# Kernel optimization log

Measured on AMD Instinct MI355X. Metric: run time of the kernel, lower is better.

Reference implementation:

```python
import jax, jax.numpy as jnp
import numpy as np

R = 16
EPS = 1e-6
OFFSETS = (1, 2, 4, 8, 16, 32)
_IDX_I, _IDX_J = np.triu_indices(R, k=1)  # plu_dim = 120


def _plucker(u, v):
    # u, v: (B, L, r) -> (B, L, plu_dim), normalized with eps-clamped norm
    p = u[..., _IDX_I] * v[..., _IDX_J] - u[..., _IDX_J] * v[..., _IDX_I]
    norm = jnp.maximum(jnp.linalg.norm(p, axis=-1, keepdims=True), EPS)
    return p / norm


def setup_inputs() -> dict:
    key = jax.random.key(0)
    ks = jax.random.split(key, 6)
    B, L, D, d_geom = 4, 4096, 1024, 256
    plu_dim = R * (R - 1) // 2
    s = lambda fan_in: 1.0 / np.sqrt(fan_in)
    return {
        "h": jax.random.normal(ks[0], (B, L, D), jnp.float32),
        "red_w": jax.random.normal(ks[1], (D, R), jnp.float32) * s(D),
        "red_b": jnp.zeros((R,), jnp.float32),
        "g1_w": jax.random.normal(ks[2], (plu_dim, d_geom), jnp.float32) * s(plu_dim),
        "g1_b": jnp.zeros((d_geom,), jnp.float32),
        "g2_w": jax.random.normal(ks[3], (d_geom, D), jnp.float32) * s(d_geom),
        "g2_b": jnp.zeros((D,), jnp.float32),
        "gate_w": jax.random.normal(ks[4], (2 * D, D), jnp.float32) * s(2 * D),
        "gate_b": jnp.zeros((D,), jnp.float32),
    }


def reference(h, red_w, red_b, g1_w, g1_b, g2_w, g2_b, gate_w, gate_b):
    B, L, D = h.shape
    z = h @ red_w + red_b  # (B, L, r)
    geom_sum = jnp.zeros((B, L, D), h.dtype)
    count = jnp.zeros((B, L, 1), h.dtype)
    pos = jnp.arange(L)
    for delta in OFFSETS:
        if delta >= L:
            continue
        # causal shift: z_past[t] = z[t - delta], zero-padded
        z_past = jnp.pad(z[:, : L - delta], ((0, 0), (delta, 0), (0, 0)))
        p = _plucker(z_past, z)  # (B, L, plu_dim)
        g_delta = jax.nn.gelu(p @ g1_w + g1_b, approximate=False) @ g2_w + g2_b
        mask = (pos >= delta).astype(h.dtype)[None, :, None]  # (1, L, 1)
        geom_sum = geom_sum + g_delta * mask
        count = count + jnp.broadcast_to(mask, (B, L, 1))
    g = geom_sum / jnp.maximum(count, 1.0)
    alpha = jax.nn.sigmoid(jnp.concatenate([h, g], axis=-1) @ gate_w + gate_b)
    return alpha * h + (1.0 - alpha) * g
```

## Files before the change

### kernel.cpp

```cpp
#include <hip/hip_runtime.h>
#include <hip/hip_bf16.h>
#include <math.h>

typedef unsigned short u16;
typedef unsigned int u32;
typedef __attribute__((ext_vector_type(8))) short short8;
typedef __attribute__((ext_vector_type(4))) float f32x4;

#define L_SEQ 4096
#define N_TOK 16384
#define D_MODEL 1024
#define R_DIM 16
#define PLU 120
#define G_DIM 256
#define K_CAT 1536
#define K_GATE 2048

typedef __attribute__((address_space(1))) const void* as1cvp;
typedef __attribute__((address_space(3))) void* as3vp;
#define GLD16(g, l) \
  __builtin_amdgcn_global_load_lds((as1cvp)(g), (as3vp)(l), 16, 0, 0)

#define CFENCE asm volatile("" ::: "memory")
#define BARB                        \
  {                                 \
    CFENCE;                         \
    __builtin_amdgcn_s_barrier();   \
    CFENCE;                         \
  }
#define VM0 asm volatile("s_waitcnt vmcnt(0)" ::: "memory")

__device__ __forceinline__ u16 f2bf(float f) {
  u32 x = __float_as_uint(f);
  u32 lsb = (x >> 16) & 1u;
  x += 0x7fffu + lsb;
  return (u16)(x >> 16);
}
__device__ __forceinline__ float bf2f(u16 u) {
  return __uint_as_float(((u32)u) << 16);
}
__device__ __forceinline__ u32 pack2(float a, float b) {
  return (u32)f2bf(a) | ((u32)f2bf(b) << 16);
}

constexpr int PLU_I[PLU] = {
    0, 0, 0, 0, 0, 0, 0, 0, 0, 0, 0, 0, 0, 0, 0,
    1, 1, 1, 1, 1, 1, 1, 1, 1, 1, 1, 1, 1, 1,
    2, 2, 2, 2, 2, 2, 2, 2, 2, 2, 2, 2, 2,
    3, 3, 3, 3, 3, 3, 3, 3, 3, 3, 3, 3,
    4, 4, 4, 4, 4, 4, 4, 4, 4, 4, 4,
    5, 5, 5, 5, 5, 5, 5, 5, 5, 5,
    6, 6, 6, 6, 6, 6, 6, 6, 6,
    7, 7, 7, 7, 7, 7, 7, 7,
    8, 8, 8, 8, 8, 8, 8,
    9, 9, 9, 9, 9, 9,
    10, 10, 10, 10, 10,
    11, 11, 11, 11,
    12, 12, 12,
    13, 13,
    14};
constexpr int PLU_J[PLU] = {
    1, 2, 3, 4, 5, 6, 7, 8, 9, 10, 11, 12, 13, 14, 15,
    2, 3, 4, 5, 6, 7, 8, 9, 10, 11, 12, 13, 14, 15,
    3, 4, 5, 6, 7, 8, 9, 10, 11, 12, 13, 14, 15,
    4, 5, 6, 7, 8, 9, 10, 11, 12, 13, 14, 15,
    5, 6, 7, 8, 9, 10, 11, 12, 13, 14, 15,
    6, 7, 8, 9, 10, 11, 12, 13, 14, 15,
    7, 8, 9, 10, 11, 12, 13, 14, 15,
    8, 9, 10, 11, 12, 13, 14, 15,
    9, 10, 11, 12, 13, 14, 15,
    10, 11, 12, 13, 14, 15,
    11, 12, 13, 14, 15,
    12, 13, 14, 15,
    13, 14, 15,
    14, 15,
    15};

__global__ __launch_bounds__(256) void k_cvtT(const float* __restrict__ src,
                                              u16* __restrict__ dst, int K,
                                              int Kp, int N) {
  __shared__ float t[32][33];
  const int k0 = blockIdx.y * 32, n0 = blockIdx.x * 32;
  const int r = threadIdx.x >> 3, c4 = (threadIdx.x & 7) * 4;
  float4 v = {0.f, 0.f, 0.f, 0.f};
  if (k0 + r < K) v = *(const float4*)(src + (size_t)(k0 + r) * N + n0 + c4);
  t[r][c4] = v.x;
  t[r][c4 + 1] = v.y;
  t[r][c4 + 2] = v.z;
  t[r][c4 + 3] = v.w;
  __syncthreads();
  uint2 o;
  o.x = pack2(t[c4][r], t[c4 + 1][r]);
  o.y = pack2(t[c4 + 2][r], t[c4 + 3][r]);
  *(uint2*)(dst + (size_t)(n0 + r) * Kp + k0 + c4) = o;
}

__global__ __launch_bounds__(256) void k_reduce(const float* __restrict__ h,
                                                const float* __restrict__ red_w,
                                                const float* __restrict__ red_b,
                                                float* __restrict__ z,
                                                u16* __restrict__ hb) {
  __shared__ alignas(16) u16 hs[16 * D_MODEL];
  const int tid = threadIdx.x;
  const int t0 = blockIdx.x * 16;

  const float4* src = (const float4*)(h + (size_t)t0 * D_MODEL);
  u32* dst = (u32*)hs;
#pragma unroll
  for (int it = 0; it < (16 * D_MODEL / 4) / 256; ++it) {
    const int idx = tid + it * 256;
    const float4 v = src[idx];
    dst[idx * 2 + 0] = pack2(v.x, v.y);
    dst[idx * 2 + 1] = pack2(v.z, v.w);
  }
  __syncthreads();

  {
    const uint4* s4 = (const uint4*)hs;
    uint4* d4 = (uint4*)(hb + (size_t)t0 * D_MODEL);
#pragma unroll
    for (int it = 0; it < (16 * D_MODEL / 8) / 256; ++it)
      d4[tid + it * 256] = s4[tid + it * 256];
  }

  const int m = tid >> 4, c = tid & 15;
  const u16* hrow = hs + m * D_MODEL;
  float acc = 0.f;
#pragma unroll 8
  for (int i = 0; i < D_MODEL; i += 2) {
    u32 hv = *(const u32*)(hrow + i);
    float h0 = __uint_as_float(hv << 16);
    float h1 = __uint_as_float(hv & 0xffff0000u);
    acc = fmaf(h0, red_w[i * R_DIM + c], acc);
    acc = fmaf(h1, red_w[(i + 1) * R_DIM + c], acc);
  }
  z[(size_t)(t0 + m) * R_DIM + c] = acc + red_b[c];
}

__global__ __launch_bounds__(256) void k_plu(const float* __restrict__ z,
                                             const u16* __restrict__ W1t,
                                             const float* __restrict__ g1b,
                                             u16* __restrict__ A, int t0g) {
  __shared__ alignas(16) float zx[160][17];
  __shared__ alignas(16) u16 W1s[128][136];
  __shared__ alignas(16) u16 Pb[128][136];
  __shared__ float prt[128][2];
  __shared__ float rno[128];
  __shared__ float b1s[128];

  const int tid = threadIdx.x, lane = tid & 63, w = tid >> 6;
  const int wm = w >> 1, wn = w & 1;
  const int n0 = blockIdx.x * 128;
  const int tl = blockIdx.y * 128;
  const int tg = t0g + tl;
  const int l0 = tg & (L_SEQ - 1);
  const int kq = (lane >> 4) * 8, mr = lane & 15;

  if (tid < 128) b1s[tid] = g1b[n0 + tid];
  for (int r = tid; r < 160 * 16; r += 256) {
    const int rr = r >> 4, c = r & 15;
    int t = tg - 32 + rr;
    if (t < 0) t = 0;
    zx[rr][c] = z[(size_t)t * R_DIM + c];
  }
  {
    const uint4* src = (const uint4*)(W1t + (size_t)n0 * 128);
    for (int i = tid; i < 128 * 16; i += 256) {
      const int r = i >> 4, c = i & 15;
      *(uint4*)&W1s[r][c * 8] = src[i];
    }
  }

  f32x4 acc[4][4];

#pragma unroll 1
  for (int dd = 0; dd < 6; ++dd) {
    const int delta = 1 << dd;
    __syncthreads();
    {
      const int row = tid >> 1, half = tid & 1;
      const float* zc = zx[32 + row];
      const float* zpr = zx[32 + row - delta];
      float zcr[R_DIM], zpr_[R_DIM];
#pragma unroll
      for (int c = 0; c < R_DIM; ++c) {
        zcr[c] = zc[c];
        zpr_[c] = zpr[c];
      }
      float s = 0.f;
      u16* pb = &Pb[row][0];
      if (half == 0) {
#pragma unroll
        for (int k = 0; k < 60; ++k) {
          const float p = zpr_[PLU_I[k]] * zcr[PLU_J[k]] -
                          zpr_[PLU_J[k]] * zcr[PLU_I[k]];
          s = fmaf(p, p, s);
          pb[k] = f2bf(p);
        }
      } else {
#pragma unroll
        for (int k = 60; k < 120; ++k) {
          const float p = zpr_[PLU_I[k]] * zcr[PLU_J[k]] -
                          zpr_[PLU_J[k]] * zcr[PLU_I[k]];
          s = fmaf(p, p, s);
          pb[k] = f2bf(p);
        }
        uint4 zz = {0u, 0u, 0u, 0u};
        *(uint4*)&pb[120] = zz;
      }
      prt[row][half] = s;
    }
    __syncthreads();
    if (tid < 128) {
      const float s = prt[tid][0] + prt[tid][1];
      rno[tid] = 1.0f / fmaxf(sqrtf(s), 1e-6f);
    }
    __syncthreads();
#pragma unroll
    for (int a = 0; a < 4; ++a)
#pragma unroll
      for (int b = 0; b < 4; ++b) acc[a][b] = (f32x4)(0.f);
#pragma unroll
    for (int k0 = 0; k0 < 128; k0 += 32) {
      short8 af[4], bfr[4];
#pragma unroll
      for (int mi = 0; mi < 4; ++mi)
        af[mi] = *(const short8*)&Pb[wm * 64 + mi * 16 + mr][k0 + kq];
#pragma unroll
      for (int ni = 0; ni < 4; ++ni)
        bfr[ni] = *(const short8*)&W1s[wn * 64 + ni * 16 + mr][k0 + kq];
#pragma unroll
      for (int mi = 0; mi < 4; ++mi)
#pragma unroll
        for (int ni = 0; ni < 4; ++ni)
          acc[mi][ni] = __builtin_amdgcn_mfma_f32_16x16x32_bf16(
              af[mi], bfr[ni], acc[mi][ni], 0, 0, 0);
    }
#pragma unroll
    for (int mi = 0; mi < 4; ++mi) {
#pragma unroll
      for (int r = 0; r < 4; ++r) {
        const int rowl = wm * 64 + mi * 16 + (lane >> 4) * 4 + r;
        const bool ok = (l0 + rowl) >= delta;
        const float rn = rno[rowl];
#pragma unroll
        for (int ni = 0; ni < 4; ++ni) {
          const int colL = wn * 64 + ni * 16 + mr;
          const float x = acc[mi][ni][r] * rn + b1s[colL];
          const float ge = 0.5f * x * (1.0f + erff(x * 0.70710678118654752f));
          A[(size_t)(tl + rowl) * K_CAT + dd * G_DIM + n0 + colL] =
              ok ? f2bf(ge) : (u16)0;
        }
      }
    }
  }
}


#define COMP(BUF)                                                             \
  {                                                                           \
    _Pragma("unroll") for (int kk = 0; kk < 2; ++kk) {                        \
      short8 af[4], bfr[4];                                                   \
      _Pragma("unroll") for (int mi = 0; mi < 4; ++mi) {                      \
        const int r = wm * 64 + mi * 16 + mr;                                 \
        af[mi] = *(const short8*)&lds[(BUF)*8192 + r * 64 +                   \
                                      (((qlane + kk * 4) ^ (r & 7)) << 3)];   \
      }                                                                       \
      _Pragma("unroll") for (int ni = 0; ni < 4; ++ni) {                      \
        const int r = wn * 64 + ni * 16 + mr;                                 \
        bfr[ni] = *(const short8*)&lds[16384 + (BUF)*8192 + r * 64 +          \
                                       (((qlane + kk * 4) ^ (r & 7)) << 3)];  \
      }                                                                       \
      _Pragma("unroll") for (int mi = 0; mi < 4; ++mi)                        \
          _Pragma("unroll") for (int ni = 0; ni < 4; ++ni) acc[mi][ni] =      \
          __builtin_amdgcn_mfma_f32_16x16x32_bf16(af[mi], bfr[ni],            \
                                                  acc[mi][ni], 0, 0, 0);      \
    }                                                                         \
  }

__global__ __launch_bounds__(256, 2) void k_gemm2(const u16* __restrict__ A,
                                                  const u16* __restrict__ W2t,
                                                  const float* __restrict__ g2b,
                                                  u16* __restrict__ g,
                                                  int t0g) {
  __shared__ alignas(16) u16 lds[32768];
  const int tid = threadIdx.x, lane = tid & 63, w = tid >> 6;
  const int wm = w >> 1, wn = w & 1;

  const int cpx = (int)gridDim.x >> 3;
  const int wi = ((int)blockIdx.x & 7) * cpx + ((int)blockIdx.x >> 3);
  const int n0 = (wi & 7) << 7;
  const int ml = (wi >> 3) << 7;

  const int lr3 = lane >> 3, lc = lane & 7;
  const int koff = (lc ^ lr3) << 3;
  const int rb = w * 32 + lr3;
  const u16* a0 = A + (size_t)(ml + rb) * K_CAT + koff;
  const u16* b0 = W2t + (size_t)(n0 + rb) * G_DIM + koff;

#define STA(BUF, T)                                                           \
  _Pragma("unroll") for (int q = 0; q < 4; ++q)                               \
      GLD16(a0 + (size_t)(q * 8) * K_CAT + (T)*64,                            \
            lds + (BUF)*8192 + (w * 32 + q * 8) * 64);
#define STB(BUF, T)                                                           \
  _Pragma("unroll") for (int q = 0; q < 4; ++q)                               \
      GLD16(b0 + (size_t)(q * 8) * G_DIM + (((T)*64) & (G_DIM - 1)),          \
            lds + 16384 + (BUF)*8192 + (w * 32 + q * 8) * 64);

  const int qlane = lane >> 4, mr = lane & 15;

  f32x4 acc[4][4];
#pragma unroll
  for (int a = 0; a < 4; ++a)
#pragma unroll
    for (int b = 0; b < 4; ++b) acc[a][b] = (f32x4)(0.f);

  const int NT = K_CAT / 64;
  STA(0, 0);
  STB(0, 0);
  VM0;
  BARB;
#pragma unroll 1
  for (int i = 0; i < NT / 2; ++i) {
    const int t1 = 2 * i + 1;
    STA(1, t1);
    STB(1, t1);
    COMP(0);
    VM0;
    BARB;
    const bool pf = (t1 + 1 < NT);
    if (pf) {
      STA(0, t1 + 1);
      STB(0, t1 + 1);
    }
    COMP(1);
    if (pf) {
      VM0;
      BARB;
    }
  }

  const int colb = n0 + wn * 64 + mr;
#pragma unroll
  for (int mi = 0; mi < 4; ++mi) {
#pragma unroll
    for (int r = 0; r < 4; ++r) {
      const int rowl = ml + wm * 64 + mi * 16 + qlane * 4 + r;
      const int l = (t0g + rowl) & (L_SEQ - 1);
      const float cnt = (float)((l >= 1) + (l >= 2) + (l >= 4) + (l >= 8) +
                                (l >= 16) + (l >= 32));
      const float inv = 1.0f / fmaxf(cnt, 1.0f);
#pragma unroll
      for (int ni = 0; ni < 4; ++ni) {
        const int col = colb + ni * 16;
        const float v = (acc[mi][ni][r] + cnt * g2b[col]) * inv;
        g[(size_t)rowl * D_MODEL + col] = f2bf(v);
      }
    }
  }
#undef STA
#undef STB
}

__global__ __launch_bounds__(256, 2) void k_gate(const u16* __restrict__ hb,
                                                 const u16* __restrict__ g,
                                                 const u16* __restrict__ WtG,
                                                 const float* __restrict__ gb,
                                                 float* __restrict__ out,
                                                 int t0g) {
  __shared__ alignas(16) u16 lds[32768];
  const int tid = threadIdx.x, lane = tid & 63, w = tid >> 6;
  const int wm = w >> 1, wn = w & 1;

  const int cpx = (int)gridDim.x >> 3;
  const int wi = ((int)blockIdx.x & 7) * cpx + ((int)blockIdx.x >> 3);
  const int n0 = (wi & 7) << 7;
  const int ml = (wi >> 3) << 7;

  const int lr3 = lane >> 3, lc = lane & 7;
  const int koff = (lc ^ lr3) << 3;
  const int rb = w * 32 + lr3;
  const u16* ph = hb + (size_t)(t0g + ml + rb) * D_MODEL + koff;
  const u16* pg = g + (size_t)(ml + rb) * D_MODEL + koff;
  const u16* pb = WtG + (size_t)(n0 + rb) * K_GATE + koff;

#define STA(BUF, T)                                                           \
  {                                                                           \
    const u16* s_ = ((T) < 16 ? ph : pg) + (size_t)((T)&15) * 64;             \
    _Pragma("unroll") for (int q = 0; q < 4; ++q)                             \
        GLD16(s_ + (size_t)(q * 8) * D_MODEL,                                 \
              lds + (BUF)*8192 + (w * 32 + q * 8) * 64);                      \
  }
#define STB(BUF, T)                                                           \
  _Pragma("unroll") for (int q = 0; q < 4; ++q)                               \
      GLD16(pb + (size_t)(q * 8) * K_GATE + (T)*64,                           \
            lds + 16384 + (BUF)*8192 + (w * 32 + q * 8) * 64);

  const int qlane = lane >> 4, mr = lane & 15;

  f32x4 acc[4][4];
#pragma unroll
  for (int a = 0; a < 4; ++a)
#pragma unroll
    for (int b = 0; b < 4; ++b) acc[a][b] = (f32x4)(0.f);

  const int NT = K_GATE / 64;
  STA(0, 0);
  STB(0, 0);
  VM0;
  BARB;
#pragma unroll 1
  for (int i = 0; i < NT / 2; ++i) {
    const int t1 = 2 * i + 1;
    STA(1, t1);
    STB(1, t1);
    COMP(0);
    VM0;
    BARB;
    const bool pf = (t1 + 1 < NT);
    if (pf) {
      STA(0, t1 + 1);
      STB(0, t1 + 1);
    }
    COMP(1);
    if (pf) {
      VM0;
      BARB;
    }
  }

  const int colb = n0 + wn * 64 + mr;
#pragma unroll
  for (int mi = 0; mi < 4; ++mi) {
#pragma unroll
    for (int r = 0; r < 4; ++r) {
      const int rowl = ml + wm * 64 + mi * 16 + qlane * 4 + r;
      const size_t rowg = (size_t)(t0g + rowl) * D_MODEL;
#pragma unroll
      for (int ni = 0; ni < 4; ++ni) {
        const int col = colb + ni * 16;
        const float x = acc[mi][ni][r] + gb[col];
        const float al = 1.0f / (1.0f + expf(-x));
        const float hv = bf2f(hb[rowg + col]);
        const float gv = bf2f(g[(size_t)rowl * D_MODEL + col]);
        out[rowg + col] = fmaf(al, hv - gv, gv);
      }
    }
  }
#undef STA
#undef STB
}

extern "C" void kernel_launch(void* const* d_in, const int* in_sizes, int n_in,
                              void* d_out, int out_size, void* d_ws,
                              size_t ws_size, hipStream_t stream) {
  const float* h = (const float*)d_in[0];
  const float* red_w = (const float*)d_in[1];
  const float* red_b = (const float*)d_in[2];
  const float* g1w = (const float*)d_in[3];
  const float* g1b = (const float*)d_in[4];
  const float* g2w = (const float*)d_in[5];
  const float* g2b = (const float*)d_in[6];
  const float* gate_w = (const float*)d_in[7];
  const float* gate_b = (const float*)d_in[8];
  float* out = (float*)d_out;

  const size_t sz_z = ((size_t)N_TOK * R_DIM * 4 + 255) & ~(size_t)255;
  const size_t sz_hb = (size_t)N_TOK * D_MODEL * 2;
  const size_t sz_WtG = (size_t)D_MODEL * K_GATE * 2;
  const size_t sz_W2t = (size_t)D_MODEL * G_DIM * 2;
  const size_t sz_W1t = (size_t)G_DIM * 128 * 2;
  const size_t fixed = sz_z + sz_hb + sz_WtG + sz_W2t + sz_W1t + 4096;

  int nc = 1;
  for (; nc <= 8; nc *= 2) {
    const size_t ct = N_TOK / nc;
    if (fixed + ct * (size_t)K_CAT * 2 + ct * (size_t)D_MODEL * 2 <= ws_size)
      break;
  }
  if (nc > 8) nc = 8;
  const int ct = N_TOK / nc;

  char* p = (char*)d_ws;
  float* z = (float*)p;
  p += sz_z;
  u16* hb = (u16*)p;
  p += sz_hb;
  u16* WtG = (u16*)p;
  p += sz_WtG;
  u16* W2t = (u16*)p;
  p += sz_W2t;
  u16* W1t = (u16*)p;
  p += sz_W1t;
  u16* Abuf = (u16*)p;
  p += (size_t)ct * K_CAT * 2;
  u16* gbuf = (u16*)p;

  k_reduce<<<dim3(N_TOK / 16), 256, 0, stream>>>(h, red_w, red_b, z, hb);
  k_cvtT<<<dim3(G_DIM / 32, 128 / 32), 256, 0, stream>>>(g1w, W1t, PLU, 128,
                                                         G_DIM);
  k_cvtT<<<dim3(D_MODEL / 32, G_DIM / 32), 256, 0, stream>>>(g2w, W2t, G_DIM,
                                                             G_DIM, D_MODEL);
  k_cvtT<<<dim3(D_MODEL / 32, K_GATE / 32), 256, 0, stream>>>(
      gate_w, WtG, K_GATE, K_GATE, D_MODEL);

  for (int c = 0; c < nc; ++c) {
    const int t0g = c * ct;
    k_plu<<<dim3(2, ct / 128), 256, 0, stream>>>(z, W1t, g1b, Abuf, t0g);
    k_gemm2<<<dim3((ct / 128) * 8), 256, 0, stream>>>(Abuf, W2t, g2b, gbuf,
                                                      t0g);
    k_gate<<<dim3((ct / 128) * 8), 256, 0, stream>>>(hb, gbuf, WtG, gate_b,
                                                     out, t0g);
  }
}
```

Measured before the change: 374.7 us.

## Double k_plu block to 512 threads and vectorize Plucker bf16 stores

The Plucker feature kernel now runs 8 waves per block instead of 4. Each row's 120 (padded to 128) Plucker coordinates are split across four thread quarters instead of two, and each quarter writes packed 16-byte bf16 stores instead of scalar u16 stores. The MFMA tile per wave is halved in the N dimension (4x2 instead of 4x4 fragments). The goal is to cut the serial Plucker compute and LDS store cost and to add latency hiding, at the price of more A-fragment LDS reads per MFMA and a 4-way norm reduction.

```diff
diff --git a/kernel.cpp b/kernel.cpp
--- a/kernel.cpp
+++ b/kernel.cpp
@@ -137,27 +137,47 @@
   z[(size_t)(t0 + m) * R_DIM + c] = acc + red_b[c];
 }
 
-__global__ __launch_bounds__(256) void k_plu(const float* __restrict__ z,
+#define PLUQ(Q)                                                               \
+  _Pragma("unroll") for (int cc = 0; cc < 4; ++cc) {                          \
+    u32 ow[4];                                                                \
+    _Pragma("unroll") for (int eo = 0; eo < 4; ++eo) {                        \
+      float pp[2];                                                            \
+      _Pragma("unroll") for (int e2 = 0; e2 < 2; ++e2) {                      \
+        const int k = ((Q)*4 + cc) * 8 + eo * 2 + e2;                         \
+        float p = 0.f;                                                        \
+        if (k < PLU) {                                                        \
+          p = zp[PLU_I[k]] * zcr[PLU_J[k]] - zp[PLU_J[k]] * zcr[PLU_I[k]];    \
+          s = fmaf(p, p, s);                                                  \
+        }                                                                     \
+        pp[e2] = p;                                                           \
+      }                                                                       \
+      ow[eo] = pack2(pp[0], pp[1]);                                           \
+    }                                                                         \
+    *(uint4*)&pb[((Q)*4 + cc) * 8] = *(uint4*)ow;                             \
+  }
+
+__global__ __launch_bounds__(512) void k_plu(const float* __restrict__ z,
                                              const u16* __restrict__ W1t,
                                              const float* __restrict__ g1b,
                                              u16* __restrict__ A, int t0g) {
   __shared__ alignas(16) float zx[160][17];
   __shared__ alignas(16) u16 W1s[128][136];
   __shared__ alignas(16) u16 Pb[128][136];
-  __shared__ float prt[128][2];
+  __shared__ float prt[128][4];
   __shared__ float rno[128];
   __shared__ float b1s[128];
 
   const int tid = threadIdx.x, lane = tid & 63, w = tid >> 6;
-  const int wm = w >> 1, wn = w & 1;
+  const int wm = w >> 2, wn = w & 3;
   const int n0 = blockIdx.x * 128;
   const int tl = blockIdx.y * 128;
   const int tg = t0g + tl;
   const int l0 = tg & (L_SEQ - 1);
   const int kq = (lane >> 4) * 8, mr = lane & 15;
+  const int qlane = lane >> 4;
 
   if (tid < 128) b1s[tid] = g1b[n0 + tid];
-  for (int r = tid; r < 160 * 16; r += 256) {
+  for (int r = tid; r < 160 * 16; r += 512) {
     const int rr = r >> 4, c = r & 15;
     int t = tg - 32 + rr;
     if (t < 0) t = 0;
@@ -165,74 +185,62 @@
   }
   {
     const uint4* src = (const uint4*)(W1t + (size_t)n0 * 128);
-    for (int i = tid; i < 128 * 16; i += 256) {
+    for (int i = tid; i < 128 * 16; i += 512) {
       const int r = i >> 4, c = i & 15;
       *(uint4*)&W1s[r][c * 8] = src[i];
     }
   }
 
-  f32x4 acc[4][4];
+  f32x4 acc[4][2];
 
 #pragma unroll 1
   for (int dd = 0; dd < 6; ++dd) {
     const int delta = 1 << dd;
     __syncthreads();
     {
-      const int row = tid >> 1, half = tid & 1;
+      const int q = w >> 1;
+      const int row = (w & 1) * 64 + lane;
       const float* zc = zx[32 + row];
       const float* zpr = zx[32 + row - delta];
-      float zcr[R_DIM], zpr_[R_DIM];
+      float zcr[R_DIM], zp[R_DIM];
 #pragma unroll
       for (int c = 0; c < R_DIM; ++c) {
         zcr[c] = zc[c];
-        zpr_[c] = zpr[c];
+        zp[c] = zpr[c];
       }
       float s = 0.f;
       u16* pb = &Pb[row][0];
-      if (half == 0) {
-#pragma unroll
-        for (int k = 0; k < 60; ++k) {
-          const float p = zpr_[PLU_I[k]] * zcr[PLU_J[k]] -
-                          zpr_[PLU_J[k]] * zcr[PLU_I[k]];
-          s = fmaf(p, p, s);
-          pb[k] = f2bf(p);
-        }
-      } else {
-#pragma unroll
-        for (int k = 60; k < 120; ++k) {
-          const float p = zpr_[PLU_I[k]] * zcr[PLU_J[k]] -
-                          zpr_[PLU_J[k]] * zcr[PLU_I[k]];
-          s = fmaf(p, p, s);
-          pb[k] = f2bf(p);
-        }
-        uint4 zz = {0u, 0u, 0u, 0u};
-        *(uint4*)&pb[120] = zz;
+      switch (q) {
+        case 0: PLUQ(0); break;
+        case 1: PLUQ(1); break;
+        case 2: PLUQ(2); break;
+        default: PLUQ(3); break;
       }
-      prt[row][half] = s;
+      prt[row][q] = s;
     }
     __syncthreads();
     if (tid < 128) {
-      const float s = prt[tid][0] + prt[tid][1];
+      const float s = prt[tid][0] + prt[tid][1] + prt[tid][2] + prt[tid][3];
       rno[tid] = 1.0f / fmaxf(sqrtf(s), 1e-6f);
     }
     __syncthreads();
 #pragma unroll
     for (int a = 0; a < 4; ++a)
 #pragma unroll
-      for (int b = 0; b < 4; ++b) acc[a][b] = (f32x4)(0.f);
+      for (int b = 0; b < 2; ++b) acc[a][b] = (f32x4)(0.f);
 #pragma unroll
     for (int k0 = 0; k0 < 128; k0 += 32) {
-      short8 af[4], bfr[4];
+      short8 af[4], bfr[2];
 #pragma unroll
       for (int mi = 0; mi < 4; ++mi)
         af[mi] = *(const short8*)&Pb[wm * 64 + mi * 16 + mr][k0 + kq];
 #pragma unroll
-      for (int ni = 0; ni < 4; ++ni)
-        bfr[ni] = *(const short8*)&W1s[wn * 64 + ni * 16 + mr][k0 + kq];
+      for (int ni = 0; ni < 2; ++ni)
+        bfr[ni] = *(const short8*)&W1s[wn * 32 + ni * 16 + mr][k0 + kq];
 #pragma unroll
       for (int mi = 0; mi < 4; ++mi)
 #pragma unroll
-        for (int ni = 0; ni < 4; ++ni)
+        for (int ni = 0; ni < 2; ++ni)
           acc[mi][ni] = __builtin_amdgcn_mfma_f32_16x16x32_bf16(
               af[mi], bfr[ni], acc[mi][ni], 0, 0, 0);
     }
@@ -240,12 +248,12 @@
     for (int mi = 0; mi < 4; ++mi) {
 #pragma unroll
       for (int r = 0; r < 4; ++r) {
-        const int rowl = wm * 64 + mi * 16 + (lane >> 4) * 4 + r;
+        const int rowl = wm * 64 + mi * 16 + qlane * 4 + r;
         const bool ok = (l0 + rowl) >= delta;
         const float rn = rno[rowl];
 #pragma unroll
-        for (int ni = 0; ni < 4; ++ni) {
-          const int colL = wn * 64 + ni * 16 + mr;
+        for (int ni = 0; ni < 2; ++ni) {
+          const int colL = wn * 32 + ni * 16 + mr;
           const float x = acc[mi][ni][r] * rn + b1s[colL];
           const float ge = 0.5f * x * (1.0f + erff(x * 0.70710678118654752f));
           A[(size_t)(tl + rowl) * K_CAT + dd * G_DIM + n0 + colL] =
@@ -506,7 +514,7 @@
 
   for (int c = 0; c < nc; ++c) {
     const int t0g = c * ct;
-    k_plu<<<dim3(2, ct / 128), 256, 0, stream>>>(z, W1t, g1b, Abuf, t0g);
+    k_plu<<<dim3(2, ct / 128), 512, 0, stream>>>(z, W1t, g1b, Abuf, t0g);
     k_gemm2<<<dim3((ct / 128) * 8), 256, 0, stream>>>(Abuf, W2t, g2b, gbuf,
                                                       t0g);
     k_gate<<<dim3((ct / 128) * 8), 256, 0, stream>>>(hb, gbuf, WtG, gate_b,
```

New measurement: 338.1 us. 1.11x faster.
